# Kernel optimization log

Hardware: AMD Instinct MI355X
Metric: run time of the kernel (lower is better)

The kernel has to match this reference:

```python
import jax, jax.numpy as jnp
import numpy as np

B, T, N, D, H = 2, 12, 1024, 128, 8
HD = D // H  # head_dim = 16


def setup_inputs() -> dict:
    key = jax.random.key(0)
    ks = jax.random.split(key, 11)
    std = 0.02
    return {
        "query": jax.random.normal(ks[0], (B, T, N, D), dtype=jnp.float32),
        "key": jax.random.normal(ks[1], (B, T, N, D), dtype=jnp.float32),
        "value": jax.random.normal(ks[2], (B, T, N, D), dtype=jnp.float32),
        "Wq": jax.random.normal(ks[3], (D, D), dtype=jnp.float32) * std,
        "bq": jnp.zeros((D,), dtype=jnp.float32),
        "Wk": jax.random.normal(ks[4], (D, D), dtype=jnp.float32) * std,
        "bk": jnp.zeros((D,), dtype=jnp.float32),
        "Wv": jax.random.normal(ks[5], (D, D), dtype=jnp.float32) * std,
        "bv": jnp.zeros((D,), dtype=jnp.float32),
        "Wo": jax.random.normal(ks[6], (D, D), dtype=jnp.float32) * std,
        "bo": jnp.zeros((D,), dtype=jnp.float32),
    }


def reference(query, key, value, Wq, bq, Wk, bk, Wv, bv, Wo, bo):
    # Linear projections (torch nn.Linear: x @ W.T + b)
    q = query @ Wq.T + bq   # (B,T,N,D)
    k = key @ Wk.T + bk
    v = value @ Wv.T + bv
    # split heads: last dim D -> (H, HD)
    q = q.reshape(B, T, N, H, HD)
    k = k.reshape(B, T, N, H, HD)
    v = v.reshape(B, T, N, H, HD)
    scale = 1.0 / jnp.sqrt(jnp.float32(HD))
    # attention across node dim (N); scores (B,H,T,N,N) ~ 805 MB
    scores = jnp.einsum('btnhd,btmhd->bhtnm', q, k) * scale
    attn = jax.nn.softmax(scores, axis=-1)
    out = jnp.einsum('bhtnm,btmhd->btnhd', attn, v)  # (B,T,N,H,HD)
    out = out.reshape(B, T, N, D)
    return out @ Wo.T + bo
```

## Files before the change

### kernel.cpp

```cpp
#include <hip/hip_runtime.h>


#define DEV __device__ __forceinline__

typedef __attribute__((ext_vector_type(4))) float f32x4;
typedef __attribute__((ext_vector_type(8))) short s16x8;
typedef __attribute__((ext_vector_type(4))) short s16x4;
typedef __attribute__((ext_vector_type(2))) unsigned int u32x2;
typedef __attribute__((ext_vector_type(4))) unsigned int u32x4;

DEV unsigned short f2bf(float f) {
    unsigned u = __builtin_bit_cast(unsigned, f);
    u = (u + 0x7fffu + ((u >> 16) & 1u)) >> 16;
    return (unsigned short)u;
}

DEV unsigned pack_bf16(float a, float b) {
#if __has_builtin(__builtin_amdgcn_cvt_pk_bf16_f32)
    typedef __attribute__((ext_vector_type(2))) __bf16 bf16x2;
    bf16x2 t = __builtin_amdgcn_cvt_pk_bf16_f32(a, b);
    return __builtin_bit_cast(unsigned, t);
#else
    unsigned ua = __builtin_bit_cast(unsigned, a) + 0x8000u;
    unsigned ub = __builtin_bit_cast(unsigned, b) + 0x8000u;
    return __builtin_amdgcn_perm(ub, ua, 0x07060302);
#endif
}

DEV f32x4 mfma16(s16x4 a, s16x4 b, f32x4 c) {
#if __has_builtin(__builtin_amdgcn_mfma_f32_16x16x16bf16_1k)
    return __builtin_amdgcn_mfma_f32_16x16x16bf16_1k(a, b, c, 0, 0, 0);
#else
    s16x8 a8 = {a[0], a[1], a[2], a[3], 0, 0, 0, 0};
    s16x8 b8 = {b[0], b[1], b[2], b[3], 0, 0, 0, 0};
    return __builtin_amdgcn_mfma_f32_16x16x32_bf16(a8, b8, c, 0, 0, 0);
#endif
}

DEV f32x4 mfma32(s16x8 a, s16x8 b, f32x4 c) {
    return __builtin_amdgcn_mfma_f32_16x16x32_bf16(a, b, c, 0, 0, 0);
}

__global__ __launch_bounds__(256)
void qkv_proj_kernel(const float* __restrict__ xq, const float* __restrict__ xk,
                     const float* __restrict__ xv,
                     const float* __restrict__ Wq, const float* __restrict__ Wk,
                     const float* __restrict__ Wv,
                     const float* __restrict__ bq, const float* __restrict__ bk,
                     const float* __restrict__ bv,
                     unsigned short* __restrict__ oq, unsigned short* __restrict__ ok,
                     unsigned short* __restrict__ ov)
{
    const int z = blockIdx.y;
    const float* X    = (z == 0) ? xq : (z == 1) ? xk : xv;
    const float* W    = (z == 0) ? Wq : (z == 1) ? Wk : Wv;
    const float* bias = (z == 0) ? bq : (z == 1) ? bk : bv;
    unsigned short* out = (z == 0) ? oq : (z == 1) ? ok : ov;
    const float scale = (z == 0) ? 0.25f * 1.44269504088896f : 1.0f;

    __shared__ unsigned short Xs[64 * 136];
    __shared__ unsigned short Ws[128 * 136];

    const int t  = threadIdx.x;
    const int m0 = blockIdx.x * 64;

    {
        const float4* Xg = (const float4*)(X + (size_t)m0 * 128);
        #pragma unroll
        for (int p = 0; p < 8; p++) {
            int g = p * 256 + t;
            float4 vv = Xg[g];
            int row = g >> 5, c4 = g & 31;
            ushort4 d;
            d.x = f2bf(vv.x); d.y = f2bf(vv.y); d.z = f2bf(vv.z); d.w = f2bf(vv.w);
            *(ushort4*)&Xs[row * 136 + c4 * 4] = d;
        }
        const float4* Wg = (const float4*)W;
        #pragma unroll
        for (int p = 0; p < 16; p++) {
            int g = p * 256 + t;
            float4 vv = Wg[g];
            int row = g >> 5, c4 = g & 31;
            ushort4 d;
            d.x = f2bf(vv.x); d.y = f2bf(vv.y); d.z = f2bf(vv.z); d.w = f2bf(vv.w);
            *(ushort4*)&Ws[row * 136 + c4 * 4] = d;
        }
    }
    __syncthreads();

    const int wave = t >> 6, lane = t & 63, quad = lane >> 4, n16 = lane & 15;
    f32x4 acc[8];
    const f32x4 zero4 = {0.f, 0.f, 0.f, 0.f};
    #pragma unroll
    for (int i = 0; i < 8; i++) acc[i] = zero4;

    #pragma unroll
    for (int ks = 0; ks < 4; ks++) {
        s16x8 a = *(const s16x8*)&Xs[(wave * 16 + n16) * 136 + ks * 32 + quad * 8];
        #pragma unroll
        for (int nt = 0; nt < 8; nt++) {
            s16x8 b = *(const s16x8*)&Ws[(nt * 16 + n16) * 136 + ks * 32 + quad * 8];
            acc[nt] = __builtin_amdgcn_mfma_f32_16x16x32_bf16(a, b, acc[nt], 0, 0, 0);
        }
    }

    const int bt    = m0 >> 10;
    const int nbase = (m0 & 1023) + wave * 16 + quad * 4;
    if (z == 2) {
        #pragma unroll
        for (int nt = 0; nt < 8; nt++) {
            float bb = bias[nt * 16 + n16];
            u32x2 pv = {pack_bf16(acc[nt][0] + bb, acc[nt][1] + bb),
                        pack_bf16(acc[nt][2] + bb, acc[nt][3] + bb)};
            *(u32x2*)&out[((size_t)(bt * 8 + nt) * 16 + n16) * 1024 + nbase] = pv;
        }
    } else {
        __syncthreads();
        const int crow = wave * 16 + quad * 4;
        #pragma unroll
        for (int nt = 0; nt < 8; nt++) {
            float bb = bias[nt * 16 + n16];
            #pragma unroll
            for (int r = 0; r < 4; r++)
                Xs[(crow + r) * 136 + nt * 16 + n16] = f2bf((acc[nt][r] + bb) * scale);
        }
        __syncthreads();
        #pragma unroll
        for (int p = 0; p < 4; p++) {
            int g = p * 256 + t, row = g >> 4, ch = g & 15;
            s16x8 val = *(const s16x8*)&Xs[row * 136 + ch * 8];
            *(s16x8*)&out[((size_t)(bt * 8 + (ch >> 1)) * 1024 + (m0 & 1023) + row) * 16
                          + (ch & 1) * 8] = val;
        }
    }
}

__global__ __launch_bounds__(256)
void attn_kernel(const unsigned short* __restrict__ q,
                 const unsigned short* __restrict__ k,
                 const unsigned short* __restrict__ vt,
                 unsigned short* __restrict__ O)
{
    __shared__ unsigned short Ks[256 * 20];
    __shared__ unsigned short VTs[16 * 264];

    const int t    = threadIdx.x;
    const int wave = t >> 6, lane = t & 63, quad = lane >> 4, n16 = lane & 15;
    const int bx = blockIdx.x, h = blockIdx.y, bt = blockIdx.z;
    const size_t headoff = (size_t)(bt * 8 + h) * 16384;
    const int q0 = bx * 64 + wave * 16;

    s16x4 qf = *(const s16x4*)(q + headoff + (size_t)(q0 + n16) * 16 + quad * 4);

    const f32x4 zero4 = {0.f, 0.f, 0.f, 0.f};
    f32x4 oacc = zero4, dacc = zero4;
    const s16x8 ones = {0x3F80, 0x3F80, 0x3F80, 0x3F80,
                        0x3F80, 0x3F80, 0x3F80, 0x3F80};
    const int krd = n16 * 20 + quad * 4;
    const int vrd = n16 * 264 + quad * 8;

    for (int c = 0; c < 4; c++) {
        __syncthreads();
        #pragma unroll
        for (int p = 0; p < 4; p++) {
            int g = p * 256 + t, rr = g >> 2, qq = g & 3;
            int r5 = rr & 31;
            int lrow = (rr & ~31) + ((r5 & 4) << 2) + ((r5 >> 3) << 2) + (r5 & 3);
            *(s16x4*)&Ks[lrow * 20 + qq * 4] =
                *(const s16x4*)(k + headoff + (size_t)(c * 256 + rr) * 16 + qq * 4);
        }
        #pragma unroll
        for (int p = 0; p < 2; p++) {
            int g = p * 256 + t, row = g >> 5, seg = g & 31;
            *(s16x8*)&VTs[row * 264 + seg * 8] =
                *(const s16x8*)(vt + headoff + (size_t)row * 1024 + c * 256 + seg * 8);
        }
        __syncthreads();

        #pragma unroll
        for (int w = 0; w < 8; w++) {
            const int jb = w * 32;
            s16x4 kf0 = *(const s16x4*)&Ks[jb * 20 + krd];
            s16x4 kf1 = *(const s16x4*)&Ks[(jb + 16) * 20 + krd];
            f32x4 s0 = mfma16(kf0, qf, zero4);
            f32x4 s1 = mfma16(kf1, qf, zero4);
            float p0 = __builtin_amdgcn_exp2f(s0[0]);
            float p1 = __builtin_amdgcn_exp2f(s0[1]);
            float p2 = __builtin_amdgcn_exp2f(s0[2]);
            float p3 = __builtin_amdgcn_exp2f(s0[3]);
            float p4 = __builtin_amdgcn_exp2f(s1[0]);
            float p5 = __builtin_amdgcn_exp2f(s1[1]);
            float p6 = __builtin_amdgcn_exp2f(s1[2]);
            float p7 = __builtin_amdgcn_exp2f(s1[3]);
            u32x4 pp = {pack_bf16(p0, p1), pack_bf16(p2, p3),
                        pack_bf16(p4, p5), pack_bf16(p6, p7)};
            s16x8 pf = __builtin_bit_cast(s16x8, pp);
            s16x8 vf = *(const s16x8*)&VTs[jb + vrd];
            oacc = mfma32(pf, vf, oacc);
            dacc = mfma32(pf, ones, dacc);
        }
    }

    const int orow = q0 + quad * 4;
    #pragma unroll
    for (int r = 0; r < 4; r++) {
        float rv = oacc[r] * __builtin_amdgcn_rcpf(dacc[r]);
        O[((size_t)bt * 1024 + orow + r) * 128 + h * 16 + n16] = f2bf(rv);
    }
}

__global__ __launch_bounds__(256)
void o_proj_kernel(const unsigned short* __restrict__ X, const float* __restrict__ W,
                   const float* __restrict__ bias, float* __restrict__ out)
{
    __shared__ unsigned short Xs[64 * 136];
    __shared__ unsigned short Ws[128 * 136];

    const int t  = threadIdx.x;
    const int m0 = blockIdx.x * 64;

    {
        #pragma unroll
        for (int p = 0; p < 4; p++) {
            int g = p * 256 + t, row = g >> 4, ch = g & 15;
            *(s16x8*)&Xs[row * 136 + ch * 8] =
                *(const s16x8*)(X + (size_t)(m0 + row) * 128 + ch * 8);
        }
        const float4* Wg = (const float4*)W;
        #pragma unroll
        for (int p = 0; p < 16; p++) {
            int g = p * 256 + t;
            float4 vv = Wg[g];
            int row = g >> 5, c4 = g & 31;
            ushort4 d;
            d.x = f2bf(vv.x); d.y = f2bf(vv.y); d.z = f2bf(vv.z); d.w = f2bf(vv.w);
            *(ushort4*)&Ws[row * 136 + c4 * 4] = d;
        }
    }
    __syncthreads();

    const int wave = t >> 6, lane = t & 63, quad = lane >> 4, n16 = lane & 15;
    f32x4 acc[8];
    const f32x4 zero4 = {0.f, 0.f, 0.f, 0.f};
    #pragma unroll
    for (int i = 0; i < 8; i++) acc[i] = zero4;

    #pragma unroll
    for (int ks = 0; ks < 4; ks++) {
        s16x8 a = *(const s16x8*)&Xs[(wave * 16 + n16) * 136 + ks * 32 + quad * 8];
        #pragma unroll
        for (int nt = 0; nt < 8; nt++) {
            s16x8 b = *(const s16x8*)&Ws[(nt * 16 + n16) * 136 + ks * 32 + quad * 8];
            acc[nt] = __builtin_amdgcn_mfma_f32_16x16x32_bf16(a, b, acc[nt], 0, 0, 0);
        }
    }

    const int mrow = m0 + wave * 16 + quad * 4;
    #pragma unroll
    for (int nt = 0; nt < 8; nt++) {
        float bb = bias[nt * 16 + n16];
        #pragma unroll
        for (int r = 0; r < 4; r++)
            out[(size_t)(mrow + r) * 128 + nt * 16 + n16] = acc[nt][r] + bb;
    }
}

extern "C" void kernel_launch(void* const* d_in, const int* in_sizes, int n_in,
                              void* d_out, int out_size, void* d_ws, size_t ws_size,
                              hipStream_t stream)
{
    const float* query = (const float*)d_in[0];
    const float* key_  = (const float*)d_in[1];
    const float* value = (const float*)d_in[2];
    const float* Wq = (const float*)d_in[3];
    const float* bq = (const float*)d_in[4];
    const float* Wk = (const float*)d_in[5];
    const float* bk = (const float*)d_in[6];
    const float* Wv = (const float*)d_in[7];
    const float* bv = (const float*)d_in[8];
    const float* Wo = (const float*)d_in[9];
    const float* bo = (const float*)d_in[10];
    float* out = (float*)d_out;

    char* ws = (char*)d_ws;
    unsigned short* qb = (unsigned short*)(ws);
    unsigned short* kb = (unsigned short*)(ws + 6291456);
    unsigned short* vb = (unsigned short*)(ws + 12582912);
    unsigned short* Ob = (unsigned short*)(ws + 18874368);

    qkv_proj_kernel<<<dim3(384, 3, 1), 256, 0, stream>>>(
        query, key_, value, Wq, Wk, Wv, bq, bk, bv, qb, kb, vb);
    attn_kernel<<<dim3(16, 8, 24), 256, 0, stream>>>(qb, kb, vb, Ob);
    o_proj_kernel<<<dim3(384, 1, 1), 256, 0, stream>>>(Ob, Wo, bo, out);
}
```

Before: 152.4 us.

## Double-buffer K/V tiles in LDS with register prefetch in attention kernel

The attention kernel now keeps two LDS buffers for K and V^T. Each iteration loads the next chunk from global memory into registers before the MFMA/exp loop and writes it to the other buffer afterwards, so only one barrier is needed per chunk instead of two. The K row swizzle also moves from the store side to the read-side address computation. The aim is to hide global load latency behind compute. The cost is about twice the shared memory and more registers, which may reduce occupancy.

```diff
diff --git a/kernel.cpp b/kernel.cpp
--- a/kernel.cpp
+++ b/kernel.cpp
@@ -141,11 +141,12 @@
                  const unsigned short* __restrict__ vt,
                  unsigned short* __restrict__ O)
 {
-    __shared__ unsigned short Ks[256 * 20];
-    __shared__ unsigned short VTs[16 * 264];
+    __shared__ unsigned short Ks[2][256 * 20];
+    __shared__ unsigned short VTs[2][16 * 264];
 
     const int t    = threadIdx.x;
-    const int wave = t >> 6, lane = t & 63, quad = lane >> 4, n16 = lane & 15;
+    const int lane = t & 63, quad = lane >> 4, n16 = lane & 15;
+    const int wave = t >> 6;
     const int bx = blockIdx.x, h = blockIdx.y, bt = blockIdx.z;
     const size_t headoff = (size_t)(bt * 8 + h) * 16384;
     const int q0 = bx * 64 + wave * 16;
@@ -156,32 +157,41 @@
     f32x4 oacc = zero4, dacc = zero4;
     const s16x8 ones = {0x3F80, 0x3F80, 0x3F80, 0x3F80,
                         0x3F80, 0x3F80, 0x3F80, 0x3F80};
-    const int krd = n16 * 20 + quad * 4;
-    const int vrd = n16 * 264 + quad * 8;
-
+    const int krd0 = (8 * (n16 >> 2) + (n16 & 3)) * 20 + quad * 4;
+    const int vrd  = n16 * 264 + quad * 8;
+    const int krow = t >> 2, kseg = (t & 3) * 4;
+    const int vrow = t >> 5, vseg = (t & 31) * 8;
+    const unsigned short* kg = k  + headoff + (size_t)krow * 16 + kseg;
+    const unsigned short* vg = vt + headoff + (size_t)vrow * 1024 + vseg;
+
+    #pragma unroll
+    for (int p = 0; p < 4; p++)
+        *(s16x4*)&Ks[0][(p * 64 + krow) * 20 + kseg] =
+            *(const s16x4*)(kg + (size_t)p * 1024);
+    #pragma unroll
+    for (int p = 0; p < 2; p++)
+        *(s16x8*)&VTs[0][(p * 8 + vrow) * 264 + vseg] =
+            *(const s16x8*)(vg + (size_t)p * 8192);
+
+    #pragma unroll
     for (int c = 0; c < 4; c++) {
         __syncthreads();
-        #pragma unroll
-        for (int p = 0; p < 4; p++) {
-            int g = p * 256 + t, rr = g >> 2, qq = g & 3;
-            int r5 = rr & 31;
-            int lrow = (rr & ~31) + ((r5 & 4) << 2) + ((r5 >> 3) << 2) + (r5 & 3);
-            *(s16x4*)&Ks[lrow * 20 + qq * 4] =
-                *(const s16x4*)(k + headoff + (size_t)(c * 256 + rr) * 16 + qq * 4);
-        }
-        #pragma unroll
-        for (int p = 0; p < 2; p++) {
-            int g = p * 256 + t, row = g >> 5, seg = g & 31;
-            *(s16x8*)&VTs[row * 264 + seg * 8] =
-                *(const s16x8*)(vt + headoff + (size_t)row * 1024 + c * 256 + seg * 8);
-        }
-        __syncthreads();
-
+        s16x4 kst[4];
+        s16x8 vst[2];
+        if (c < 3) {
+            #pragma unroll
+            for (int p = 0; p < 4; p++)
+                kst[p] = *(const s16x4*)(kg + (size_t)((c + 1) * 256 + p * 64) * 16);
+            #pragma unroll
+            for (int p = 0; p < 2; p++)
+                vst[p] = *(const s16x8*)(vg + (c + 1) * 256 + (size_t)p * 8192);
+        }
+        const unsigned short* Kc = Ks[c & 1];
+        const unsigned short* Vc = VTs[c & 1];
         #pragma unroll
         for (int w = 0; w < 8; w++) {
-            const int jb = w * 32;
-            s16x4 kf0 = *(const s16x4*)&Ks[jb * 20 + krd];
-            s16x4 kf1 = *(const s16x4*)&Ks[(jb + 16) * 20 + krd];
+            s16x4 kf0 = *(const s16x4*)&Kc[w * 640 + krd0];
+            s16x4 kf1 = *(const s16x4*)&Kc[w * 640 + krd0 + 80];
             f32x4 s0 = mfma16(kf0, qf, zero4);
             f32x4 s1 = mfma16(kf1, qf, zero4);
             float p0 = __builtin_amdgcn_exp2f(s0[0]);
@@ -195,9 +205,19 @@
             u32x4 pp = {pack_bf16(p0, p1), pack_bf16(p2, p3),
                         pack_bf16(p4, p5), pack_bf16(p6, p7)};
             s16x8 pf = __builtin_bit_cast(s16x8, pp);
-            s16x8 vf = *(const s16x8*)&VTs[jb + vrd];
+            s16x8 vf = *(const s16x8*)&Vc[w * 32 + vrd];
             oacc = mfma32(pf, vf, oacc);
             dacc = mfma32(pf, ones, dacc);
+        }
+        if (c < 3) {
+            unsigned short* Kn = Ks[(c + 1) & 1];
+            unsigned short* Vn = VTs[(c + 1) & 1];
+            #pragma unroll
+            for (int p = 0; p < 4; p++)
+                *(s16x4*)&Kn[(p * 64 + krow) * 20 + kseg] = kst[p];
+            #pragma unroll
+            for (int p = 0; p < 2; p++)
+                *(s16x8*)&Vn[(p * 8 + vrow) * 264 + vseg] = vst[p];
         }
     }
 
```

New measurement: 146.6 us. 1.04x faster.
